# Kernel optimization log

Measured on AMD Instinct MI355X. Metric: run time of the kernel, lower is better.

Reference implementation:

```python
import jax, jax.numpy as jnp
import numpy as np

B, C, H, W = 4, 256, 64, 64
C8 = C // 8


def setup_inputs() -> dict:
    key = jax.random.key(0)
    ks = jax.random.split(key, 9)
    s_in = 1.0 / np.sqrt(C)
    return {
        "x": jax.random.normal(ks[0], (B, C, H, W), dtype=jnp.float32),
        "Wq": jax.random.normal(ks[1], (C8, C), dtype=jnp.float32) * s_in,
        "bq": jax.random.normal(ks[2], (C8,), dtype=jnp.float32) * 0.01,
        "Wk": jax.random.normal(ks[3], (C8, C), dtype=jnp.float32) * s_in,
        "bk": jax.random.normal(ks[4], (C8,), dtype=jnp.float32) * 0.01,
        "Wv": jax.random.normal(ks[5], (C, C), dtype=jnp.float32) * s_in,
        "bv": jax.random.normal(ks[6], (C,), dtype=jnp.float32) * 0.01,
        "Wo": jax.random.normal(ks[7], (C, C), dtype=jnp.float32) * s_in,
        "bo": jax.random.normal(ks[8], (C,), dtype=jnp.float32) * 0.01,
    }


def reference(x, Wq, bq, Wk, bk, Wv, bv, Wo, bo):
    b, c, h, w = x.shape
    n = h * w
    xf = x.reshape(b, c, n)                                   # (B, C, N)
    # 1x1 convs are channel GEMMs
    q = jnp.einsum('bcn,dc->bnd', xf, Wq) + bq                # (B, N, C8)
    k = jnp.einsum('bcn,dc->bdn', xf, Wk) + bk[:, None]       # (B, C8, N)
    v = jnp.einsum('bcn,dc->bdn', xf, Wv) + bv[:, None]       # (B, C, N)
    energy = jnp.einsum('bnd,bdm->bnm', q, k)                 # (B, N, N)
    attn = jax.nn.softmax(energy, axis=-1)
    # out[b,c,i] = sum_j v[b,c,j] * attn[b,i,j]
    out = jnp.einsum('bcj,bij->bci', v, attn)                 # (B, C, N)
    out = out.reshape(b, c, h, w) + x                         # residual
    out = jnp.einsum('bchw,dc->bdhw', out, Wo) + bo[None, :, None, None]
    return out
```

## Files before the change

kernel.cpp:

```cpp
#include <hip/hip_runtime.h>

#define DEV __device__ __forceinline__

constexpr int B_  = 4;
constexpr int C_  = 256;
constexpr int C8_ = 32;
constexpr int N_  = 4096;
constexpr float LOG2E = 1.4426950408889634f;

using u16 = unsigned short;
using u32 = unsigned int;

typedef __attribute__((ext_vector_type(8))) short bf16x8;
typedef __attribute__((ext_vector_type(4))) float f32x4;

DEV float bf2f(u16 u) { return __uint_as_float(((u32)u) << 16); }
DEV u16   f2bf(float f) {
  u32 i = __float_as_uint(f);
  i += 0x7fffu + ((i >> 16) & 1u);
  return (u16)(i >> 16);
}
DEV u32 pack_rtz(float a, float b) {
  return __builtin_amdgcn_perm(__float_as_uint(b), __float_as_uint(a), 0x07060302);
}

DEV void lds_barrier() {
  asm volatile("s_waitcnt lgkmcnt(0)\n\ts_barrier" ::: "memory");
}

__global__ __launch_bounds__(256) void wsplit(
    const float* __restrict__ Wq, const float* __restrict__ Wk,
    const float* __restrict__ Wv, const float* __restrict__ Wo,
    u16* __restrict__ WqH, u16* __restrict__ WqL,
    u16* __restrict__ WkH, u16* __restrict__ WkL,
    u16* __restrict__ WvH,
    u16* __restrict__ WoH, u16* __restrict__ WoL)
{
  int i = blockIdx.x * 256 + threadIdx.x;
  if (i < 8192) {
    float v = Wq[i] * LOG2E;
    u16 h = f2bf(v); WqH[i] = h; WqL[i] = f2bf(v - bf2f(h));
  } else if (i < 16384) {
    int off = i - 8192;
    float v = Wk[off];
    u16 h = f2bf(v); WkH[off] = h; WkL[off] = f2bf(v - bf2f(h));
  } else if (i < 81920) {
    int off = i - 16384;
    WvH[off] = f2bf(Wv[off]);
  } else {
    int off = i - 81920;
    float v = Wo[off];
    u16 h = f2bf(v); WoH[off] = h; WoL[off] = f2bf(v - bf2f(h));
  }
}

__global__ __launch_bounds__(256) void xprep(
    const float* __restrict__ x, u16* __restrict__ xTh, u16* __restrict__ xTl)
{
  __shared__ float tf[64][65];
  const int tid = threadIdx.x;
  const int b = blockIdx.z, c0 = blockIdx.y * 64, n0 = blockIdx.x * 64;
  const int nl = tid & 63, cb = tid >> 6;

  #pragma unroll
  for (int cc = 0; cc < 16; ++cc) {
    int cl = cb * 16 + cc;
    tf[nl][cl] = x[((size_t)b * C_ + c0 + cl) * N_ + n0 + nl];
  }
  __syncthreads();

  #pragma unroll
  for (int it = 0; it < 2; ++it) {
    int idx = tid + it * 256;
    int n = idx >> 3, q = idx & 7;
    u32 ph[4], pl[4];
    #pragma unroll
    for (int j = 0; j < 4; ++j) {
      float v0 = tf[n][q * 8 + 2 * j], v1 = tf[n][q * 8 + 2 * j + 1];
      u16 h0 = f2bf(v0), h1 = f2bf(v1);
      ph[j] = (u32)h0 | ((u32)h1 << 16);
      pl[j] = (u32)f2bf(v0 - bf2f(h0)) | ((u32)f2bf(v1 - bf2f(h1)) << 16);
    }
    size_t off = ((size_t)b * N_ + n0 + n) * C_ + c0 + q * 8;
    *(uint4*)&xTh[off] = make_uint4(ph[0], ph[1], ph[2], ph[3]);
    *(uint4*)&xTl[off] = make_uint4(pl[0], pl[1], pl[2], pl[3]);
  }
}

__global__ __launch_bounds__(256) void qkv_mfma(
    const u16* __restrict__ xTh, const u16* __restrict__ xTl,
    const u16* __restrict__ WqH, const u16* __restrict__ WqL,
    const u16* __restrict__ WkH, const u16* __restrict__ WkL,
    const u16* __restrict__ WvH,
    const float* __restrict__ bq, const float* __restrict__ bk,
    const float* __restrict__ bv,
    u16* __restrict__ qt, u16* __restrict__ kt, u16* __restrict__ vb)
{
  __shared__ __align__(16) u16 xsh[32][270];
  __shared__ __align__(16) u16 xsl[32][270];

  const int tid = threadIdx.x;
  const int lane = tid & 63, w = tid >> 6, m = lane & 15, quad = lane >> 4;
  const int b = blockIdx.y, n0 = blockIdx.x * 32;

  #pragma unroll
  for (int it = 0; it < 4; ++it) {
    int chunk = tid + it * 256;
    int row = chunk >> 5, col = (chunk & 31) * 8;
    size_t g = ((size_t)b * N_ + n0 + row) * C_ + col;
    *(uint4*)&xsh[row][col] = *(const uint4*)(xTh + g);
    *(uint4*)&xsl[row][col] = *(const uint4*)(xTl + g);
  }
  __syncthreads();

  const u16* qkH = (w < 2) ? (WqH + (size_t)(w * 16 + m) * C_)
                           : (WkH + (size_t)((w - 2) * 16 + m) * C_);
  const u16* qkL = (w < 2) ? (WqL + (size_t)(w * 16 + m) * C_)
                           : (WkL + (size_t)((w - 2) * 16 + m) * C_);

  f32x4 ov[4][2], oq[2];
  #pragma unroll
  for (int dt = 0; dt < 4; ++dt)
    #pragma unroll
    for (int nt = 0; nt < 2; ++nt) ov[dt][nt] = (f32x4){0.f, 0.f, 0.f, 0.f};
  #pragma unroll
  for (int nt = 0; nt < 2; ++nt) oq[nt] = (f32x4){0.f, 0.f, 0.f, 0.f};

  for (int K = 0; K < 8; ++K) {
    const int ko = K * 32 + quad * 8;
    bf16x8 xh[2], xl[2];
    #pragma unroll
    for (int nt = 0; nt < 2; ++nt) {
      xh[nt] = *(const bf16x8*)&xsh[nt * 16 + m][ko];
      xl[nt] = *(const bf16x8*)&xsl[nt * 16 + m][ko];
    }
    #pragma unroll
    for (int dt = 0; dt < 4; ++dt) {
      bf16x8 whi = *(const bf16x8*)(WvH + (size_t)(64 * w + dt * 16 + m) * C_ + ko);
      #pragma unroll
      for (int nt = 0; nt < 2; ++nt)
        ov[dt][nt] = __builtin_amdgcn_mfma_f32_16x16x32_bf16(whi, xh[nt], ov[dt][nt], 0, 0, 0);
    }
    {
      bf16x8 bhi = *(const bf16x8*)(qkH + ko);
      bf16x8 blo = *(const bf16x8*)(qkL + ko);
      #pragma unroll
      for (int nt = 0; nt < 2; ++nt) {
        oq[nt] = __builtin_amdgcn_mfma_f32_16x16x32_bf16(xh[nt], bhi, oq[nt], 0, 0, 0);
        oq[nt] = __builtin_amdgcn_mfma_f32_16x16x32_bf16(xl[nt], bhi, oq[nt], 0, 0, 0);
        oq[nt] = __builtin_amdgcn_mfma_f32_16x16x32_bf16(xh[nt], blo, oq[nt], 0, 0, 0);
      }
    }
  }

  #pragma unroll
  for (int dt = 0; dt < 4; ++dt)
    #pragma unroll
    for (int r = 0; r < 4; ++r) {
      int oc = 64 * w + dt * 16 + quad * 4 + r;
      float bias = bv[oc];
      #pragma unroll
      for (int nt = 0; nt < 2; ++nt)
        vb[((size_t)b * C_ + oc) * N_ + n0 + nt * 16 + m] = f2bf(ov[dt][nt][r] + bias);
    }
  {
    u16* qk_out = (w < 2) ? qt : kt;
    int dbase = (w & 1) * 16;
    float bias = (w < 2) ? bq[dbase + m] * LOG2E : bk[dbase + m];
    #pragma unroll
    for (int nt = 0; nt < 2; ++nt)
      #pragma unroll
      for (int r = 0; r < 4; ++r)
        qk_out[((size_t)b * N_ + n0 + nt * 16 + quad * 4 + r) * C8_ + dbase + m] =
            f2bf(oq[nt][r] + bias);
  }
}

__global__ __launch_bounds__(256) void attn_mfma(
    const u16* __restrict__ qt, const u16* __restrict__ kt,
    const u16* __restrict__ vb,
    u16* __restrict__ Onorm, float* __restrict__ ml)
{
  __shared__ __align__(16) u16  ps[2][64][136];
  __shared__ __align__(16) float als[2][64];
  __shared__ float lfin[64];

  const int tid = threadIdx.x, lane = tid & 63, w = tid >> 6;
  const int m = lane & 15, quad = lane >> 4;

  const int lid = blockIdx.x + gridDim.x * (blockIdx.y + gridDim.y * blockIdx.z);
  const int grp = lid & 15, ksl = grp & 3, b = grp >> 2;
  const int i0 = (lid >> 4) * 64;

  const bf16x8 qfrag =
      *(const bf16x8*)(qt + ((size_t)b * N_ + i0 + w * 16 + m) * C8_ + quad * 8);
  const u16* kbase = kt + (size_t)b * N_ * C8_;
  const u16* vrow  = vb + ((size_t)b * C_ + w * 64 + m) * N_;

  f32x4 o[4][4];
  #pragma unroll
  for (int t = 0; t < 4; ++t)
    #pragma unroll
    for (int ct = 0; ct < 4; ++ct) o[t][ct] = (f32x4){0.f, 0.f, 0.f, 0.f};
  float m_r = -1e30f, l_r = 0.f;

  const int jbeg = ksl * 1024, jend = jbeg + 1024;
  int buf = 0;

  for (int j0 = jbeg; j0 < jend; j0 += 128, buf ^= 1) {
    bf16x8 kA[8];
    #pragma unroll
    for (int t = 0; t < 8; ++t)
      kA[t] = *(const bf16x8*)(kbase + (size_t)(j0 + t * 16 + m) * C8_ + quad * 8);
    bf16x8 vB[4][4];
    #pragma unroll
    for (int ct = 0; ct < 4; ++ct)
      #pragma unroll
      for (int kk = 0; kk < 4; ++kk)
        vB[ct][kk] = *(const bf16x8*)(vrow + (size_t)ct * 16 * N_ + j0 + kk * 32 + quad * 8);

    f32x4 s[8];
    #pragma unroll
    for (int t = 0; t < 8; ++t)
      s[t] = __builtin_amdgcn_mfma_f32_16x16x32_bf16(
          kA[t], qfrag, (f32x4){0.f, 0.f, 0.f, 0.f}, 0, 0, 0);

    float mx = -1e30f;
    #pragma unroll
    for (int t = 0; t < 8; ++t)
      #pragma unroll
      for (int r = 0; r < 4; ++r) mx = fmaxf(mx, s[t][r]);
    mx = fmaxf(mx, __shfl_xor(mx, 16));
    mx = fmaxf(mx, __shfl_xor(mx, 32));
    float mn = fmaxf(m_r, mx);
    float al = exp2f(m_r - mn);
    m_r = mn;
    float p[8][4], sm = 0.f;
    #pragma unroll
    for (int t = 0; t < 8; ++t)
      #pragma unroll
      for (int r = 0; r < 4; ++r) {
        p[t][r] = exp2f(s[t][r] - mn);
        sm += p[t][r];
      }
    sm += __shfl_xor(sm, 16);
    sm += __shfl_xor(sm, 32);
    l_r = l_r * al + sm;

    #pragma unroll
    for (int t = 0; t < 8; ++t)
      *(uint2*)&ps[buf][w * 16 + m][t * 16 + quad * 4] =
          make_uint2(pack_rtz(p[t][0], p[t][1]), pack_rtz(p[t][2], p[t][3]));
    if (quad == 0) als[buf][w * 16 + m] = al;

    lds_barrier();

    #pragma unroll
    for (int t = 0; t < 4; ++t) {
      float4 alv = *(const float4*)&als[buf][t * 16 + quad * 4];
      #pragma unroll
      for (int ct = 0; ct < 4; ++ct) {
        o[t][ct][0] *= alv.x; o[t][ct][1] *= alv.y;
        o[t][ct][2] *= alv.z; o[t][ct][3] *= alv.w;
      }
    }

    #pragma unroll
    for (int t = 0; t < 4; ++t) {
      #pragma unroll
      for (int kk = 0; kk < 4; ++kk) {
        bf16x8 pf = *(const bf16x8*)&ps[buf][t * 16 + m][kk * 32 + quad * 8];
        #pragma unroll
        for (int ct = 0; ct < 4; ++ct)
          o[t][ct] = __builtin_amdgcn_mfma_f32_16x16x32_bf16(pf, vB[ct][kk], o[t][ct], 0, 0, 0);
      }
    }
  }

  if (quad == 0) lfin[w * 16 + m] = 1.f / l_r;
  lds_barrier();

  u16* Ob = Onorm + (((size_t)ksl * B_ + b) * N_ + i0) * C_ + w * 64;
  #pragma unroll
  for (int t = 0; t < 4; ++t) {
    float4 lv = *(const float4*)&lfin[t * 16 + quad * 4];
    float linv[4] = {lv.x, lv.y, lv.z, lv.w};
    #pragma unroll
    for (int ct = 0; ct < 4; ++ct)
      #pragma unroll
      for (int r = 0; r < 4; ++r)
        Ob[(size_t)(t * 16 + quad * 4 + r) * C_ + ct * 16 + m] = f2bf(o[t][ct][r] * linv[r]);
  }

  if (quad == 0) {
    size_t mli = ((size_t)ksl * B_ + b) * N_ + i0 + w * 16 + m;
    ml[mli] = m_r;
    ml[(size_t)4 * B_ * N_ + mli] = l_r;
  }
}

__global__ __launch_bounds__(256) void out_mfma(
    const u16* __restrict__ Onorm, const float* __restrict__ ml,
    const u16* __restrict__ xTh,
    const u16* __restrict__ WoH, const u16* __restrict__ WoL,
    const float* __restrict__ bo, float* __restrict__ out)
{
  __shared__ __align__(16) u16 hs[32][270];

  const int tid = threadIdx.x;
  const int lane = tid & 63, w = tid >> 6, m = lane & 15, quad = lane >> 4;
  const int b = blockIdx.y, n0 = blockIdx.x * 32;
  constexpr size_t BN = (size_t)B_ * N_;

  #pragma unroll
  for (int it = 0; it < 4; ++it) {
    int chunk = tid + it * 256;
    int row = chunk >> 5, col = (chunk & 31) * 8;
    size_t nrow = (size_t)b * N_ + n0 + row;

    float mm0 = ml[nrow], mm1 = ml[BN + nrow], mm2 = ml[2 * BN + nrow], mm3 = ml[3 * BN + nrow];
    float M = fmaxf(fmaxf(mm0, mm1), fmaxf(mm2, mm3));
    float ws[4];
    ws[0] = ml[4 * BN + nrow] * exp2f(mm0 - M);
    ws[1] = ml[5 * BN + nrow] * exp2f(mm1 - M);
    ws[2] = ml[6 * BN + nrow] * exp2f(mm2 - M);
    ws[3] = ml[7 * BN + nrow] * exp2f(mm3 - M);
    float inv = 1.f / (ws[0] + ws[1] + ws[2] + ws[3]);
    #pragma unroll
    for (int s = 0; s < 4; ++s) ws[s] *= inv;

    uint4 xv = *(const uint4*)(xTh + nrow * C_ + col);
    u32 xq[4] = {xv.x, xv.y, xv.z, xv.w};
    float acc[8];
    #pragma unroll
    for (int j = 0; j < 4; ++j) {
      acc[2 * j]     = bf2f((u16)(xq[j] & 0xffff));
      acc[2 * j + 1] = bf2f((u16)(xq[j] >> 16));
    }
    #pragma unroll
    for (int s = 0; s < 4; ++s) {
      uint4 ovv = *(const uint4*)(Onorm + (s * BN + nrow) * C_ + col);
      u32 oq[4] = {ovv.x, ovv.y, ovv.z, ovv.w};
      #pragma unroll
      for (int j = 0; j < 4; ++j) {
        acc[2 * j]     += ws[s] * bf2f((u16)(oq[j] & 0xffff));
        acc[2 * j + 1] += ws[s] * bf2f((u16)(oq[j] >> 16));
      }
    }
    uint4 pk;
    pk.x = (u32)f2bf(acc[0]) | ((u32)f2bf(acc[1]) << 16);
    pk.y = (u32)f2bf(acc[2]) | ((u32)f2bf(acc[3]) << 16);
    pk.z = (u32)f2bf(acc[4]) | ((u32)f2bf(acc[5]) << 16);
    pk.w = (u32)f2bf(acc[6]) | ((u32)f2bf(acc[7]) << 16);
    *(uint4*)&hs[row][col] = pk;
  }
  __syncthreads();

  f32x4 o[4][2];
  #pragma unroll
  for (int dt = 0; dt < 4; ++dt)
    #pragma unroll
    for (int nt = 0; nt < 2; ++nt) o[dt][nt] = (f32x4){0.f, 0.f, 0.f, 0.f};

  for (int K = 0; K < 8; ++K) {
    const int ko = K * 32 + quad * 8;
    bf16x8 hf[2];
    #pragma unroll
    for (int nt = 0; nt < 2; ++nt) hf[nt] = *(const bf16x8*)&hs[nt * 16 + m][ko];
    #pragma unroll
    for (int dt = 0; dt < 4; ++dt) {
      bf16x8 whi = *(const bf16x8*)(WoH + (size_t)(64 * w + dt * 16 + m) * C_ + ko);
      bf16x8 wlo = *(const bf16x8*)(WoL + (size_t)(64 * w + dt * 16 + m) * C_ + ko);
      #pragma unroll
      for (int nt = 0; nt < 2; ++nt) {
        o[dt][nt] = __builtin_amdgcn_mfma_f32_16x16x32_bf16(whi, hf[nt], o[dt][nt], 0, 0, 0);
        o[dt][nt] = __builtin_amdgcn_mfma_f32_16x16x32_bf16(wlo, hf[nt], o[dt][nt], 0, 0, 0);
      }
    }
  }

  #pragma unroll
  for (int dt = 0; dt < 4; ++dt)
    #pragma unroll
    for (int r = 0; r < 4; ++r) {
      int d = 64 * w + dt * 16 + quad * 4 + r;
      float bias = bo[d];
      #pragma unroll
      for (int nt = 0; nt < 2; ++nt)
        out[((size_t)b * C_ + d) * N_ + n0 + nt * 16 + m] = o[dt][nt][r] + bias;
    }
}

extern "C" void kernel_launch(void* const* d_in, const int* in_sizes, int n_in,
                              void* d_out, int out_size, void* d_ws, size_t ws_size,
                              hipStream_t stream)
{
  const float* x  = (const float*)d_in[0];
  const float* Wq = (const float*)d_in[1];
  const float* bq = (const float*)d_in[2];
  const float* Wk = (const float*)d_in[3];
  const float* bk = (const float*)d_in[4];
  const float* Wv = (const float*)d_in[5];
  const float* bv = (const float*)d_in[6];
  const float* Wo = (const float*)d_in[7];
  const float* bo = (const float*)d_in[8];

  u16* p = (u16*)d_ws;
  u16* qt  = p;  p += (size_t)B_ * N_ * C8_;
  u16* kt  = p;  p += (size_t)B_ * N_ * C8_;
  u16* vb  = p;  p += (size_t)B_ * C_ * N_;
  u16* xTh = p;  p += (size_t)B_ * N_ * C_;
  u16* WqH = p;  p += 8192;
  u16* WqL = p;  p += 8192;
  u16* WkH = p;  p += 8192;
  u16* WkL = p;  p += 8192;
  u16* WvH = p;  p += 65536;
  u16* WoH = p;  p += 65536;
  u16* WoL = p;  p += 65536;
  float* ml = (float*)p;  p += (size_t)16 * B_ * N_;
  u16* xTl   = p;
  u16* Onorm = p;

  float* out = (float*)d_out;

  wsplit<<<576, 256, 0, stream>>>(Wq, Wk, Wv, Wo,
      WqH, WqL, WkH, WkL, WvH, WoH, WoL);
  xprep<<<dim3(N_ / 64, C_ / 64, B_), 256, 0, stream>>>(x, xTh, xTl);
  qkv_mfma<<<dim3(N_ / 32, B_), 256, 0, stream>>>(
      xTh, xTl, WqH, WqL, WkH, WkL, WvH, bq, bk, bv, qt, kt, vb);
  attn_mfma<<<dim3(N_ / 64, 4, B_), 256, 0, stream>>>(qt, kt, vb, Onorm, ml);
  out_mfma<<<dim3(N_ / 32, B_), 256, 0, stream>>>(Onorm, ml, xTh, WoH, WoL, bo, out);
}
```

Measured before the change: 212.5 us.

## Halve qkv/out tile width and split attention loads into staged halves

The qkv and output-projection kernels now handle 16 spatial positions per block instead of 32, which doubles the grid size and reduces per-thread accumulators and shared memory. The attention inner loop splits K and V loads into two halves, and a sched_barrier separates the first P·V MFMA half from the second V load. This is meant to lower register pressure and raise occupancy, with some load latency hidden behind MFMA work. The cost is that weight fragments are re-read from global memory by twice as many blocks, and each block does less MFMA work relative to its overhead.

```diff
diff --git a/kernel.cpp b/kernel.cpp
--- a/kernel.cpp
+++ b/kernel.cpp
@@ -96,15 +96,15 @@
     const float* __restrict__ bv,
     u16* __restrict__ qt, u16* __restrict__ kt, u16* __restrict__ vb)
 {
-  __shared__ __align__(16) u16 xsh[32][270];
-  __shared__ __align__(16) u16 xsl[32][270];
+  __shared__ __align__(16) u16 xsh[16][270];
+  __shared__ __align__(16) u16 xsl[16][270];
 
   const int tid = threadIdx.x;
   const int lane = tid & 63, w = tid >> 6, m = lane & 15, quad = lane >> 4;
-  const int b = blockIdx.y, n0 = blockIdx.x * 32;
-
-  #pragma unroll
-  for (int it = 0; it < 4; ++it) {
+  const int b = blockIdx.y, n0 = blockIdx.x * 16;
+
+  #pragma unroll
+  for (int it = 0; it < 2; ++it) {
     int chunk = tid + it * 256;
     int row = chunk >> 5, col = (chunk & 31) * 8;
     size_t g = ((size_t)b * N_ + n0 + row) * C_ + col;
@@ -118,38 +118,26 @@
   const u16* qkL = (w < 2) ? (WqL + (size_t)(w * 16 + m) * C_)
                            : (WkL + (size_t)((w - 2) * 16 + m) * C_);
 
-  f32x4 ov[4][2], oq[2];
-  #pragma unroll
-  for (int dt = 0; dt < 4; ++dt)
-    #pragma unroll
-    for (int nt = 0; nt < 2; ++nt) ov[dt][nt] = (f32x4){0.f, 0.f, 0.f, 0.f};
-  #pragma unroll
-  for (int nt = 0; nt < 2; ++nt) oq[nt] = (f32x4){0.f, 0.f, 0.f, 0.f};
+  f32x4 ov[4], oq;
+  #pragma unroll
+  for (int dt = 0; dt < 4; ++dt) ov[dt] = (f32x4){0.f, 0.f, 0.f, 0.f};
+  oq = (f32x4){0.f, 0.f, 0.f, 0.f};
 
   for (int K = 0; K < 8; ++K) {
     const int ko = K * 32 + quad * 8;
-    bf16x8 xh[2], xl[2];
-    #pragma unroll
-    for (int nt = 0; nt < 2; ++nt) {
-      xh[nt] = *(const bf16x8*)&xsh[nt * 16 + m][ko];
-      xl[nt] = *(const bf16x8*)&xsl[nt * 16 + m][ko];
-    }
+    bf16x8 xh = *(const bf16x8*)&xsh[m][ko];
+    bf16x8 xl = *(const bf16x8*)&xsl[m][ko];
     #pragma unroll
     for (int dt = 0; dt < 4; ++dt) {
       bf16x8 whi = *(const bf16x8*)(WvH + (size_t)(64 * w + dt * 16 + m) * C_ + ko);
-      #pragma unroll
-      for (int nt = 0; nt < 2; ++nt)
-        ov[dt][nt] = __builtin_amdgcn_mfma_f32_16x16x32_bf16(whi, xh[nt], ov[dt][nt], 0, 0, 0);
+      ov[dt] = __builtin_amdgcn_mfma_f32_16x16x32_bf16(whi, xh, ov[dt], 0, 0, 0);
     }
     {
       bf16x8 bhi = *(const bf16x8*)(qkH + ko);
       bf16x8 blo = *(const bf16x8*)(qkL + ko);
-      #pragma unroll
-      for (int nt = 0; nt < 2; ++nt) {
-        oq[nt] = __builtin_amdgcn_mfma_f32_16x16x32_bf16(xh[nt], bhi, oq[nt], 0, 0, 0);
-        oq[nt] = __builtin_amdgcn_mfma_f32_16x16x32_bf16(xl[nt], bhi, oq[nt], 0, 0, 0);
-        oq[nt] = __builtin_amdgcn_mfma_f32_16x16x32_bf16(xh[nt], blo, oq[nt], 0, 0, 0);
-      }
+      oq = __builtin_amdgcn_mfma_f32_16x16x32_bf16(xh, bhi, oq, 0, 0, 0);
+      oq = __builtin_amdgcn_mfma_f32_16x16x32_bf16(xl, bhi, oq, 0, 0, 0);
+      oq = __builtin_amdgcn_mfma_f32_16x16x32_bf16(xh, blo, oq, 0, 0, 0);
     }
   }
 
@@ -158,21 +146,16 @@
     #pragma unroll
     for (int r = 0; r < 4; ++r) {
       int oc = 64 * w + dt * 16 + quad * 4 + r;
-      float bias = bv[oc];
-      #pragma unroll
-      for (int nt = 0; nt < 2; ++nt)
-        vb[((size_t)b * C_ + oc) * N_ + n0 + nt * 16 + m] = f2bf(ov[dt][nt][r] + bias);
+      vb[((size_t)b * C_ + oc) * N_ + n0 + m] = f2bf(ov[dt][r] + bv[oc]);
     }
   {
     u16* qk_out = (w < 2) ? qt : kt;
     int dbase = (w & 1) * 16;
     float bias = (w < 2) ? bq[dbase + m] * LOG2E : bk[dbase + m];
     #pragma unroll
-    for (int nt = 0; nt < 2; ++nt)
-      #pragma unroll
-      for (int r = 0; r < 4; ++r)
-        qk_out[((size_t)b * N_ + n0 + nt * 16 + quad * 4 + r) * C8_ + dbase + m] =
-            f2bf(oq[nt][r] + bias);
+    for (int r = 0; r < 4; ++r)
+      qk_out[((size_t)b * N_ + n0 + quad * 4 + r) * C8_ + dbase + m] =
+          f2bf(oq[r] + bias);
   }
 }
 
@@ -208,21 +191,27 @@
   int buf = 0;
 
   for (int j0 = jbeg; j0 < jend; j0 += 128, buf ^= 1) {
-    bf16x8 kA[8];
-    #pragma unroll
-    for (int t = 0; t < 8; ++t)
+    f32x4 s[8];
+    bf16x8 kA[4];
+    #pragma unroll
+    for (int t = 0; t < 4; ++t)
       kA[t] = *(const bf16x8*)(kbase + (size_t)(j0 + t * 16 + m) * C8_ + quad * 8);
-    bf16x8 vB[4][4];
+    #pragma unroll
+    for (int t = 0; t < 4; ++t)
+      s[t] = __builtin_amdgcn_mfma_f32_16x16x32_bf16(
+          kA[t], qfrag, (f32x4){0.f, 0.f, 0.f, 0.f}, 0, 0, 0);
+    bf16x8 vB[4][2];
     #pragma unroll
     for (int ct = 0; ct < 4; ++ct)
       #pragma unroll
-      for (int kk = 0; kk < 4; ++kk)
+      for (int kk = 0; kk < 2; ++kk)
         vB[ct][kk] = *(const bf16x8*)(vrow + (size_t)ct * 16 * N_ + j0 + kk * 32 + quad * 8);
-
-    f32x4 s[8];
-    #pragma unroll
-    for (int t = 0; t < 8; ++t)
-      s[t] = __builtin_amdgcn_mfma_f32_16x16x32_bf16(
+    #pragma unroll
+    for (int t = 0; t < 4; ++t)
+      kA[t] = *(const bf16x8*)(kbase + (size_t)(j0 + (t + 4) * 16 + m) * C8_ + quad * 8);
+    #pragma unroll
+    for (int t = 0; t < 4; ++t)
+      s[t + 4] = __builtin_amdgcn_mfma_f32_16x16x32_bf16(
           kA[t], qfrag, (f32x4){0.f, 0.f, 0.f, 0.f}, 0, 0, 0);
 
     float mx = -1e30f;
@@ -266,15 +255,32 @@
     }
 
     #pragma unroll
-    for (int t = 0; t < 4; ++t) {
-      #pragma unroll
-      for (int kk = 0; kk < 4; ++kk) {
+    for (int kk = 0; kk < 2; ++kk)
+      #pragma unroll
+      for (int t = 0; t < 4; ++t) {
         bf16x8 pf = *(const bf16x8*)&ps[buf][t * 16 + m][kk * 32 + quad * 8];
         #pragma unroll
         for (int ct = 0; ct < 4; ++ct)
           o[t][ct] = __builtin_amdgcn_mfma_f32_16x16x32_bf16(pf, vB[ct][kk], o[t][ct], 0, 0, 0);
       }
-    }
+
+    __builtin_amdgcn_sched_barrier(0);
+
+    #pragma unroll
+    for (int ct = 0; ct < 4; ++ct)
+      #pragma unroll
+      for (int kk = 0; kk < 2; ++kk)
+        vB[ct][kk] = *(const bf16x8*)(vrow + (size_t)ct * 16 * N_ + j0 + (kk + 2) * 32 + quad * 8);
+
+    #pragma unroll
+    for (int kk = 0; kk < 2; ++kk)
+      #pragma unroll
+      for (int t = 0; t < 4; ++t) {
+        bf16x8 pf = *(const bf16x8*)&ps[buf][t * 16 + m][(kk + 2) * 32 + quad * 8];
+        #pragma unroll
+        for (int ct = 0; ct < 4; ++ct)
+          o[t][ct] = __builtin_amdgcn_mfma_f32_16x16x32_bf16(pf, vB[ct][kk], o[t][ct], 0, 0, 0);
+      }
   }
 
   if (quad == 0) lfin[w * 16 + m] = 1.f / l_r;
@@ -305,15 +311,15 @@
     const u16* __restrict__ WoH, const u16* __restrict__ WoL,
     const float* __restrict__ bo, float* __restrict__ out)
 {
-  __shared__ __align__(16) u16 hs[32][270];
+  __shared__ __align__(16) u16 hs[16][270];
 
   const int tid = threadIdx.x;
   const int lane = tid & 63, w = tid >> 6, m = lane & 15, quad = lane >> 4;
-  const int b = blockIdx.y, n0 = blockIdx.x * 32;
+  const int b = blockIdx.y, n0 = blockIdx.x * 16;
   constexpr size_t BN = (size_t)B_ * N_;
 
   #pragma unroll
-  for (int it = 0; it < 4; ++it) {
+  for (int it = 0; it < 2; ++it) {
     int chunk = tid + it * 256;
     int row = chunk >> 5, col = (chunk & 31) * 8;
     size_t nrow = (size_t)b * N_ + n0 + row;
@@ -356,26 +362,19 @@
   }
   __syncthreads();
 
-  f32x4 o[4][2];
-  #pragma unroll
-  for (int dt = 0; dt < 4; ++dt)
-    #pragma unroll
-    for (int nt = 0; nt < 2; ++nt) o[dt][nt] = (f32x4){0.f, 0.f, 0.f, 0.f};
+  f32x4 o[4];
+  #pragma unroll
+  for (int dt = 0; dt < 4; ++dt) o[dt] = (f32x4){0.f, 0.f, 0.f, 0.f};
 
   for (int K = 0; K < 8; ++K) {
     const int ko = K * 32 + quad * 8;
-    bf16x8 hf[2];
-    #pragma unroll
-    for (int nt = 0; nt < 2; ++nt) hf[nt] = *(const bf16x8*)&hs[nt * 16 + m][ko];
+    bf16x8 hf = *(const bf16x8*)&hs[m][ko];
     #pragma unroll
     for (int dt = 0; dt < 4; ++dt) {
       bf16x8 whi = *(const bf16x8*)(WoH + (size_t)(64 * w + dt * 16 + m) * C_ + ko);
       bf16x8 wlo = *(const bf16x8*)(WoL + (size_t)(64 * w + dt * 16 + m) * C_ + ko);
-      #pragma unroll
-      for (int nt = 0; nt < 2; ++nt) {
-        o[dt][nt] = __builtin_amdgcn_mfma_f32_16x16x32_bf16(whi, hf[nt], o[dt][nt], 0, 0, 0);
-        o[dt][nt] = __builtin_amdgcn_mfma_f32_16x16x32_bf16(wlo, hf[nt], o[dt][nt], 0, 0, 0);
-      }
+      o[dt] = __builtin_amdgcn_mfma_f32_16x16x32_bf16(whi, hf, o[dt], 0, 0, 0);
+      o[dt] = __builtin_amdgcn_mfma_f32_16x16x32_bf16(wlo, hf, o[dt], 0, 0, 0);
     }
   }
 
@@ -384,10 +383,7 @@
     #pragma unroll
     for (int r = 0; r < 4; ++r) {
       int d = 64 * w + dt * 16 + quad * 4 + r;
-      float bias = bo[d];
-      #pragma unroll
-      for (int nt = 0; nt < 2; ++nt)
-        out[((size_t)b * C_ + d) * N_ + n0 + nt * 16 + m] = o[dt][nt][r] + bias;
+      out[((size_t)b * C_ + d) * N_ + n0 + m] = o[dt][r] + bo[d];
     }
 }
 
@@ -426,8 +422,8 @@
   wsplit<<<576, 256, 0, stream>>>(Wq, Wk, Wv, Wo,
       WqH, WqL, WkH, WkL, WvH, WoH, WoL);
   xprep<<<dim3(N_ / 64, C_ / 64, B_), 256, 0, stream>>>(x, xTh, xTl);
-  qkv_mfma<<<dim3(N_ / 32, B_), 256, 0, stream>>>(
+  qkv_mfma<<<dim3(N_ / 16, B_), 256, 0, stream>>>(
       xTh, xTl, WqH, WqL, WkH, WkL, WvH, bq, bk, bv, qt, kt, vb);
   attn_mfma<<<dim3(N_ / 64, 4, B_), 256, 0, stream>>>(qt, kt, vb, Onorm, ml);
-  out_mfma<<<dim3(N_ / 32, B_), 256, 0, stream>>>(Onorm, ml, xTh, WoH, WoL, bo, out);
-}
+  out_mfma<<<dim3(N_ / 16, B_), 256, 0, stream>>>(Onorm, ml, xTh, WoH, WoL, bo, out);
+}
```

After: 230.2 us. 8.4% more time.
